# Performance work log

Hardware: AMD Instinct MI355X
Metric: run time of the kernel (lower is better)

## Reference

```python
import jax, jax.numpy as jnp
import numpy as np

NUM_STEPS = 50
NUM_DOF = 1
NVAR = NUM_STEPS * NUM_DOF
T = 0.05
V_MAX, A_MAX, J_MAX = 1.0, 2.0, 5.0
P_MAX = np.pi
THETA0 = 0.0
RHO = 1.0
MAXITER = 15
BATCH = 32768
HIDDEN = 1024
EPS = 1e-5


def _build_mats():
    # finite-difference operators (num_dof=1 so kron with eye(1) is identity)
    P_vel = np.eye(NUM_STEPS)
    P_acc = np.diff(P_vel, axis=0) / T          # (49, 50)
    P_jerk = np.diff(P_acc, axis=0) / T         # (48, 50)
    P_pos = np.cumsum(P_vel, axis=0) * T        # (50, 50)
    A_control = np.vstack([P_vel, -P_vel, P_acc, -P_acc,
                           P_jerk, -P_jerk, P_pos, -P_pos]).astype(np.float32)  # (394, 50)
    A_eq = np.zeros((2, NUM_STEPS), np.float32)
    A_eq[0, 0] = 1.0
    A_eq[1, -1] = 1.0
    cost = np.eye(NVAR) + RHO * A_control.T @ A_control
    Q = np.block([[cost, A_eq.T], [A_eq, np.zeros((2, 2))]])
    Q_inv = np.linalg.inv(Q).astype(np.float32)  # (52, 52)
    na = NUM_STEPS - 1
    nj = na - 1
    # limits used inside the iteration (p_max on both halves)
    b_iter = np.concatenate([np.full(2 * NUM_STEPS, V_MAX), np.full(2 * na, A_MAX),
                             np.full(2 * nj, J_MAX), np.full(2 * NUM_STEPS, P_MAX)]).astype(np.float32)
    # limits used for the slack init (p_max -/+ theta_init)
    b_init = np.concatenate([np.full(2 * NUM_STEPS, V_MAX), np.full(2 * na, A_MAX),
                             np.full(2 * nj, J_MAX), np.full(NUM_STEPS, P_MAX - THETA0),
                             np.full(NUM_STEPS, P_MAX + THETA0)]).astype(np.float32)
    return jnp.asarray(A_control), jnp.asarray(Q_inv), jnp.asarray(b_iter), jnp.asarray(b_init)


def _bn(x, g, b):
    # BatchNorm1d in training mode: biased batch statistics
    m = jnp.mean(x, axis=0)
    v = jnp.var(x, axis=0)
    return g * (x - m) * jax.lax.rsqrt(v + EPS) + b


def setup_inputs() -> dict:
    key = jax.random.key(0)
    ks = jax.random.split(key, 6)
    x = jax.random.normal(ks[0], (BATCH, NVAR), jnp.float32)
    W1 = jax.random.normal(ks[1], (NVAR, HIDDEN), jnp.float32) * 0.1
    W2 = jax.random.normal(ks[2], (HIDDEN, HIDDEN), jnp.float32) * 0.03
    W3 = jax.random.normal(ks[3], (HIDDEN, 256), jnp.float32) * 0.03
    W4 = jax.random.normal(ks[4], (256, 2 * NVAR), jnp.float32) * 0.06
    z = lambda n: jnp.zeros((n,), jnp.float32)
    o = lambda n: jnp.ones((n,), jnp.float32)
    return {"xi_samples_input_nn": x,
            "W1": W1, "b1": z(HIDDEN), "g1": o(HIDDEN), "be1": z(HIDDEN),
            "W2": W2, "b2": z(HIDDEN), "g2": o(HIDDEN), "be2": z(HIDDEN),
            "W3": W3, "b3": z(256), "g3": o(256), "be3": z(256),
            "W4": W4, "b4": z(2 * NVAR)}


def reference(xi_samples_input_nn, W1, b1, g1, be1, W2, b2, g2, be2,
              W3, b3, g3, be3, W4, b4):
    x = xi_samples_input_nn  # (B, nvar): both MLP input and projection target
    A_c, Q_inv, b_it, b_in = _build_mats()

    # MLP decoder
    h = jax.nn.relu(_bn(x @ W1 + b1, g1, be1))
    h = jax.nn.relu(_bn(h @ W2 + b2, g2, be2))
    h = jax.nn.relu(_bn(h @ W3 + b3, g3, be3))
    out = h @ W4 + b4                     # (B, 2*nvar)
    xi0 = out[:, :NVAR]
    lam0 = out[:, NVAR:2 * NVAR]

    s0 = jnp.maximum(0.0, b_in - xi0 @ A_c.T)        # (B, 394)
    b_eq = jnp.zeros((x.shape[0], 2), x.dtype)       # v_start = v_goal = 0

    def step(carry, _):
        xi, s, lam = carry
        b_aug = b_it - s
        # A_projection = I, so A_proj.T @ x.T -> x
        lincost = -lam - x - RHO * (b_aug @ A_c)
        rhs = jnp.concatenate([-lincost, b_eq], axis=1)   # (B, 52)
        sol = rhs @ Q_inv.T
        xi_n = sol[:, :NVAR]
        s_n = jnp.maximum(0.0, b_it - xi_n @ A_c.T)
        res = xi_n @ A_c.T - b_it + s_n
        res_norm = jnp.linalg.norm(res, axis=1)
        lam_n = lam - RHO * (res @ A_c)
        fp = (jnp.linalg.norm(xi - xi_n, axis=1)
              + jnp.linalg.norm(lam - lam_n, axis=1)
              + jnp.linalg.norm(s - s_n, axis=1))
        return (xi_n, s_n, lam_n), (res_norm, fp)

    (xi, s, lam), (primal, fixed_pt) = jax.lax.scan(step, (xi0, s0, lam0), None, length=MAXITER)
    avg_res_fixed_point = jnp.mean(fixed_pt, axis=0)  # (B,)
    avg_res_primal = jnp.mean(primal, axis=0)         # (B,)
    return xi, avg_res_fixed_point, avg_res_primal
```

## Files before the change

### kernel.cpp

```cpp
#include <hip/hip_runtime.h>
#include <math.h>

#define BATCH 32768
#define NVARS 50
#define H1 1024
#define H2 1024
#define H3 256
#define NOUT 100
#define EPSBN 1e-5f

#define TF   0.05f
#define AF   20.0f
#define JF   400.0f
#define VMAX 1.0f
#define AMAX 2.0f
#define JMAX 5.0f
#define PMAX 3.14159265358979323846f

typedef unsigned short ushort_t;
typedef __attribute__((ext_vector_type(8))) short short8;
typedef __attribute__((ext_vector_type(4))) float f32x4;

__device__ float g_z1[(size_t)BATCH * H1];
__device__ float g_z2[(size_t)BATCH * H2];
__device__ float g_ps[32 * 1024];
__device__ float g_pq[32 * 1024];
__device__ float g_scale[3 * 1024];
__device__ float g_shift[3 * 1024];
__device__ float g_Mp[2800];
__device__ float g_xT[(size_t)NVARS * BATCH];
__device__ float g_nnT[(size_t)NOUT * BATCH];
__device__ ushort_t g_w2p[(size_t)3 * H1 * H2];
__device__ ushort_t g_w3p[(size_t)3 * H2 * H3];

__device__ __forceinline__ void split3(float f, ushort_t& h, ushort_t& m, ushort_t& l)
{
    unsigned u = __float_as_uint(f);
    unsigned r = u + 0x7fffu + ((u >> 16) & 1u);
    h = (ushort_t)(r >> 16);
    float f1 = f - __uint_as_float((unsigned)h << 16);
    unsigned u1 = __float_as_uint(f1);
    unsigned r1 = u1 + 0x7fffu + ((u1 >> 16) & 1u);
    m = (ushort_t)(r1 >> 16);
    float f2 = f1 - __uint_as_float((unsigned)m << 16);
    unsigned u2 = __float_as_uint(f2);
    unsigned r2 = u2 + 0x7fffu + ((u2 >> 16) & 1u);
    l = (ushort_t)(r2 >> 16);
}

__global__ void build_M(float* __restrict__ Mout)
{
    __shared__ double aug[52][104];
    __shared__ int piv;
    int tid = threadIdx.x;

    const double Tf = (double)0.05f;
    const double c3[3] = { 400.0, -800.0, 400.0 };

    for (int idx = tid; idx < 52 * 104; idx += 64) {
        int j = idx / 104, k = idx % 104;
        double v = 0.0;
        if (k >= 52) {
            v = (k == 52 + j) ? 1.0 : 0.0;
        } else if (j < 50 && k < 50) {
            double q = (j == k) ? 3.0 : 0.0;
            if (j == k) q += 800.0 * ((j < 49 ? 1 : 0) + (j > 0 ? 1 : 0));
            if (j - k == 1 || k - j == 1) q += -800.0;
            int lo = j > k ? j : k; lo -= 2; if (lo < 0) lo = 0;
            int hi = j < k ? j : k; if (hi > 47) hi = 47;
            for (int i = lo; i <= hi; ++i) {
                int dj = j - i, dk = k - i;
                if (dj >= 0 && dj <= 2 && dk >= 0 && dk <= 2)
                    q += 2.0 * c3[dj] * c3[dk];
            }
            int mx = j > k ? j : k;
            q += 2.0 * Tf * Tf * (double)(50 - mx);
            v = q;
        } else if ((j == 50 && k == 0) || (j == 0 && k == 50) ||
                   (j == 51 && k == 49) || (j == 49 && k == 51)) {
            v = 1.0;
        }
        aug[j][k] = v;
    }
    __syncthreads();

    for (int c = 0; c < 52; ++c) {
        if (tid == 0) {
            int p = c; double best = fabs(aug[c][c]);
            for (int r = c + 1; r < 52; ++r) {
                double v = fabs(aug[r][c]);
                if (v > best) { best = v; p = r; }
            }
            piv = p;
        }
        __syncthreads();
        int p = piv;
        if (p != c) {
            for (int k = tid; k < 104; k += 64) {
                double t = aug[c][k]; aug[c][k] = aug[p][k]; aug[p][k] = t;
            }
        }
        __syncthreads();
        double pv = aug[c][c];
        __syncthreads();
        for (int k = tid; k < 104; k += 64) aug[c][k] /= pv;
        __syncthreads();
        if (tid < 52 && tid != c) {
            double f = aug[tid][c];
            for (int k = 0; k < 104; ++k) aug[tid][k] -= f * aug[c][k];
        }
        __syncthreads();
    }

    for (int idx = tid; idx < 2800; idx += 64) {
        int slot = idx % 28;
        int kk2 = idx / 28;
        int k = kk2 >> 1, par = kk2 & 1;
        int j = par * 25 + slot;
        Mout[idx] = (slot < 25) ? (float)aug[j][52 + k] : 0.f;
    }
}

template <int C>
__global__ __launch_bounds__(64)
void transp(const float* __restrict__ Z, float* __restrict__ ZT)
{
    __shared__ float t[64][C + 1];
    const int lane = threadIdx.x;
    const size_t r0 = (size_t)blockIdx.x * 64;
#pragma unroll 1
    for (int i = 0; i < C; ++i) {
        int idx = i * 64 + lane;
        int r = idx / C, c = idx % C;
        t[r][c] = Z[r0 * C + idx];
    }
    __syncthreads();
#pragma unroll 1
    for (int c = 0; c < C; ++c)
        ZT[(size_t)c * BATCH + r0 + lane] = t[lane][c];
}

__global__ __launch_bounds__(512)
void wsplit_pack(const float* __restrict__ W, ushort_t* __restrict__ Wp,
                 int K, int N)
{
    int t = threadIdx.x;
    int n0 = blockIdx.x * 16, k0 = blockIdx.y * 32;
    int kk = t >> 4, nn = t & 15;
    float f = W[(size_t)(k0 + kk) * N + n0 + nn];
    ushort_t h, m, l;
    split3(f, h, m, l);
    int Nsub = N >> 4;
    int lane = (kk >> 3) * 16 + nn, e = kk & 7;
    size_t base = ((size_t)((k0 >> 5) * Nsub + (n0 >> 4)) * 3) * 512 + lane * 8 + e;
    Wp[base]        = h;
    Wp[base + 512]  = m;
    Wp[base + 1024] = l;
}

__global__ __launch_bounds__(256)
void gemm_mfma(const float* __restrict__ A, const ushort_t* __restrict__ Wp,
               const float* __restrict__ bias,
               const float* __restrict__ scale, const float* __restrict__ shift,
               float* __restrict__ C, int M, int K, int N, int ntn)
{
    __shared__ __attribute__((aligned(16))) ushort_t lds[3][4][64][8];

    const int nwg = gridDim.x;
    const int chunk = nwg >> 3;
    const int b = blockIdx.x;
    const int logical = (b & 7) * chunk + (b >> 3);
    const int rowt = logical / ntn;
    const int colt = logical - rowt * ntn;
    const int row0 = rowt * 64;
    const int col0s = colt * 16;

    const int t = threadIdx.x;
    const int lane = t & 63, wn = t >> 6;
    const int fr = lane & 15, fg = lane >> 4;
    const int srow = t & 63, skc = t >> 6;
    const int Nsub = N >> 4;

    f32x4 acc[4][4];
#pragma unroll
    for (int m = 0; m < 4; ++m)
#pragma unroll
        for (int n = 0; n < 4; ++n)
#pragma unroll
            for (int q = 0; q < 4; ++q) acc[m][n][q] = 0.f;

    int ks = 0;
    for (int k0 = 0; k0 < K; k0 += 32, ++ks) {
        {
            const float* ap = A + (size_t)(row0 + srow) * K + k0 + skc * 8;
            float4 f0 = *(const float4*)ap;
            float4 f1 = *(const float4*)(ap + 4);
            const float* scp = scale + k0 + skc * 8;
            const float* shp = shift + k0 + skc * 8;
            float4 sc0 = *(const float4*)scp, sc1 = *(const float4*)(scp + 4);
            float4 sh0 = *(const float4*)shp, sh1 = *(const float4*)(shp + 4);
            float v[8];
            v[0] = fmaxf(f0.x * sc0.x + sh0.x, 0.f);
            v[1] = fmaxf(f0.y * sc0.y + sh0.y, 0.f);
            v[2] = fmaxf(f0.z * sc0.z + sh0.z, 0.f);
            v[3] = fmaxf(f0.w * sc0.w + sh0.w, 0.f);
            v[4] = fmaxf(f1.x * sc1.x + sh1.x, 0.f);
            v[5] = fmaxf(f1.y * sc1.y + sh1.y, 0.f);
            v[6] = fmaxf(f1.z * sc1.z + sh1.z, 0.f);
            v[7] = fmaxf(f1.w * sc1.w + sh1.w, 0.f);
            ushort_t h_[8], m_[8], l_[8];
#pragma unroll
            for (int q = 0; q < 8; ++q) split3(v[q], h_[q], m_[q], l_[q]);
#define PK(a,b2) (((unsigned)(a)) | (((unsigned)(b2)) << 16))
            *(uint4*)&lds[0][skc][srow][0] = make_uint4(PK(h_[0],h_[1]), PK(h_[2],h_[3]), PK(h_[4],h_[5]), PK(h_[6],h_[7]));
            *(uint4*)&lds[1][skc][srow][0] = make_uint4(PK(m_[0],m_[1]), PK(m_[2],m_[3]), PK(m_[4],m_[5]), PK(m_[6],m_[7]));
            *(uint4*)&lds[2][skc][srow][0] = make_uint4(PK(l_[0],l_[1]), PK(l_[2],l_[3]), PK(l_[4],l_[5]), PK(l_[6],l_[7]));
#undef PK
        }
        __syncthreads();

        short8 b_h[4], b_m[4], b_l[4];
#pragma unroll
        for (int n = 0; n < 4; ++n) {
            size_t base = ((size_t)(ks * Nsub + col0s + wn * 4 + n) * 3) * 512 + lane * 8;
            b_h[n] = *(const short8*)(Wp + base);
            b_m[n] = *(const short8*)(Wp + base + 512);
            b_l[n] = *(const short8*)(Wp + base + 1024);
        }
#pragma unroll
        for (int m = 0; m < 4; ++m) {
            int r = m * 16 + fr;
            short8 a_h = *(const short8*)&lds[0][fg][r][0];
            short8 a_m = *(const short8*)&lds[1][fg][r][0];
            short8 a_l = *(const short8*)&lds[2][fg][r][0];
#pragma unroll
            for (int n = 0; n < 4; ++n) {
                f32x4 c = acc[m][n];
                c = __builtin_amdgcn_mfma_f32_16x16x32_bf16(a_l, b_h[n], c, 0, 0, 0);
                c = __builtin_amdgcn_mfma_f32_16x16x32_bf16(a_h, b_l[n], c, 0, 0, 0);
                c = __builtin_amdgcn_mfma_f32_16x16x32_bf16(a_m, b_m[n], c, 0, 0, 0);
                c = __builtin_amdgcn_mfma_f32_16x16x32_bf16(a_m, b_h[n], c, 0, 0, 0);
                c = __builtin_amdgcn_mfma_f32_16x16x32_bf16(a_h, b_m[n], c, 0, 0, 0);
                c = __builtin_amdgcn_mfma_f32_16x16x32_bf16(a_h, b_h[n], c, 0, 0, 0);
                acc[m][n] = c;
            }
        }
        __syncthreads();
    }

#pragma unroll
    for (int m = 0; m < 4; ++m)
#pragma unroll
        for (int n = 0; n < 4; ++n) {
            int cc = (col0s + wn * 4 + n) * 16 + fr;
            float bv = bias[cc];
#pragma unroll
            for (int q = 0; q < 4; ++q) {
                int rr = row0 + m * 16 + fg * 4 + q;
                C[(size_t)rr * N + cc] = acc[m][n][q] + bv;
            }
        }
}

template <int BN_APPLY>
__global__ __launch_bounds__(256)
void gemm_k(const float* __restrict__ A, const float* __restrict__ W,
            const float* __restrict__ bias,
            const float* __restrict__ scale, const float* __restrict__ shift,
            float* __restrict__ C, int M, int K, int N)
{
    const int BM = 128, BN = 128, BK = 16;
    __shared__ __attribute__((aligned(16))) float As[BK][BM + 4];
    __shared__ __attribute__((aligned(16))) float Ws[BK][BN];
    int tid = threadIdx.x;
    int tm = tid >> 4, tn = tid & 15;
    int row0 = blockIdx.x * BM, col0 = blockIdx.y * BN;

    float acc[8][8];
#pragma unroll
    for (int i = 0; i < 8; ++i)
#pragma unroll
        for (int j = 0; j < 8; ++j) acc[i][j] = 0.f;

    int alr = tid >> 4;
    int alk = tid & 15;
    int wlc = tid & 127;
    int wlk = tid >> 7;

    for (int k0 = 0; k0 < K; k0 += BK) {
#pragma unroll
        for (int i = 0; i < 8; ++i) {
            int rr = row0 + alr + i * 16;
            int kk = k0 + alk;
            float v = 0.f;
            if (kk < K) {
                v = A[(size_t)rr * K + kk];
                if (BN_APPLY) v = fmaxf(v * scale[kk] + shift[kk], 0.f);
            }
            As[alk][alr + i * 16] = v;
        }
#pragma unroll
        for (int i = 0; i < 8; ++i) {
            int kk = k0 + wlk + i * 2;
            int cc = col0 + wlc;
            Ws[wlk + i * 2][wlc] = (kk < K && cc < N) ? W[(size_t)kk * N + cc] : 0.f;
        }
        __syncthreads();
#pragma unroll
        for (int kk = 0; kk < BK; ++kk) {
            float av[8], wv[8];
            float4 tv;
            tv = *(const float4*)&As[kk][tm * 8];     av[0]=tv.x; av[1]=tv.y; av[2]=tv.z; av[3]=tv.w;
            tv = *(const float4*)&As[kk][tm * 8 + 4]; av[4]=tv.x; av[5]=tv.y; av[6]=tv.z; av[7]=tv.w;
            tv = *(const float4*)&Ws[kk][tn * 8];     wv[0]=tv.x; wv[1]=tv.y; wv[2]=tv.z; wv[3]=tv.w;
            tv = *(const float4*)&Ws[kk][tn * 8 + 4]; wv[4]=tv.x; wv[5]=tv.y; wv[6]=tv.z; wv[7]=tv.w;
#pragma unroll
            for (int i = 0; i < 8; ++i)
#pragma unroll
                for (int j = 0; j < 8; ++j) acc[i][j] += av[i] * wv[j];
        }
        __syncthreads();
    }
#pragma unroll
    for (int i = 0; i < 8; ++i) {
        int rr = row0 + tm * 8 + i;
#pragma unroll
        for (int j = 0; j < 8; ++j) {
            int cc = col0 + tn * 8 + j;
            if (cc < N) C[(size_t)rr * N + cc] = acc[i][j] + bias[cc];
        }
    }
}

__global__ __launch_bounds__(256)
void stats_part(const float* __restrict__ Z, float* __restrict__ ps,
                float* __restrict__ pq, int M, int C, int chunks)
{
    int lc = threadIdx.x & 63;
    int col = blockIdx.x * 64 + lc;
    int rg = threadIdx.x >> 6;
    int rpc = M / chunks;
    int r0 = blockIdx.y * rpc;
    float s = 0.f, q = 0.f;
    for (int rr = r0 + rg; rr < r0 + rpc; rr += 4) {
        float v = Z[(size_t)rr * C + col];
        s += v; q += v * v;
    }
    __shared__ float ls[4][64], lq[4][64];
    ls[rg][lc] = s; lq[rg][lc] = q;
    __syncthreads();
    if (rg == 0) {
        float S = ls[0][lc] + ls[1][lc] + ls[2][lc] + ls[3][lc];
        float Q = lq[0][lc] + lq[1][lc] + lq[2][lc] + lq[3][lc];
        ps[(size_t)blockIdx.y * C + col] = S;
        pq[(size_t)blockIdx.y * C + col] = Q;
    }
}

__global__ void stats_fin(const float* __restrict__ ps, const float* __restrict__ pq,
                          const float* __restrict__ g, const float* __restrict__ be,
                          float* __restrict__ scale, float* __restrict__ shift,
                          int C, int M, int chunks)
{
    int c = blockIdx.x * blockDim.x + threadIdx.x;
    if (c >= C) return;
    float S = 0.f, Q = 0.f;
    for (int i = 0; i < chunks; ++i) { S += ps[(size_t)i * C + c]; Q += pq[(size_t)i * C + c]; }
    float inv = 1.0f / (float)M;
    float mean = S * inv;
    float var = Q * inv - mean * mean;
    float rstd = 1.0f / sqrtf(var + EPSBN);
    float sc = g[c] * rstd;
    scale[c] = sc;
    shift[c] = be[c] - mean * sc;
}

__global__ __launch_bounds__(64, 1)
void iter_k(const float* __restrict__ XT, const float* __restrict__ NNT,
            const float* __restrict__ Mp, float* __restrict__ out)
{
    __shared__ float sA[50 * 32];
    __shared__ float sB[50 * 32];
    __shared__ float sLam[50 * 32];
    __shared__ float sXv[50 * 32];
    __shared__ float sRh[50 * 32];
    const int lane = threadIdx.x;
    const int r = lane >> 1, par = lane & 1;
    const int base = blockIdx.x * 32;
    const int row = base + r;
#define IDX2(k) (((k) << 5) + r)

#pragma unroll 1
    for (int idx = lane; idx < 1600; idx += 64) {
        int k = idx >> 5, rr = idx & 31;
        sA[idx]   = NNT[(size_t)k * BATCH + base + rr];
        sLam[idx] = NNT[(size_t)(50 + k) * BATCH + base + rr];
        sXv[idx]  = XT[(size_t)k * BATCH + base + rr];
    }
    float* cx = sA;
    float* cn = sB;
    float fps = 0.f, prs = 0.f;
    float rh[50];
    const float* mp = Mp + par * 28;

#pragma unroll 1
    for (int it = 0; it < 15; ++it) {
#pragma unroll
        for (int k = 0; k < 50; ++k) rh[k] = 0.f;
        {
            float pre = 0.f, Sp = 0.f, ap = 0.f;
            float xc = cx[IDX2(0)];
#pragma unroll
            for (int k = 0; k < 50; ++k) {
                float xn = (k < 49) ? cx[IDX2(k + 1)] : 0.f;
                rh[k] += fminf(VMAX, xc) - fminf(VMAX, -xc);
                rh[k] -= TF * Sp;
                pre += xc;
                float p = TF * pre;
                Sp += fminf(PMAX, p) - fminf(PMAX, -p);
                if (k < 49) {
                    float a = AF * (xn - xc);
                    float da = fminf(AMAX, a) - fminf(AMAX, -a);
                    rh[k] -= AF * da; rh[k + 1] += AF * da;
                    if (k >= 1) {
                        float j = AF * (a - ap);
                        float dj = fminf(JMAX, j) - fminf(JMAX, -j);
                        rh[k - 1] += JF * dj; rh[k] -= 2.f * JF * dj; rh[k + 1] += JF * dj;
                    }
                    ap = a;
                }
                xc = xn;
            }
            float Stot = TF * Sp;
#pragma unroll
            for (int k = 0; k < 50; ++k)
                sRh[IDX2(k)] = rh[k] + sLam[IDX2(k)] + sXv[IDX2(k)] + Stot;
        }

        {
            float xr[28];
#pragma unroll
            for (int jj = 0; jj < 28; ++jj) xr[jj] = 0.f;
#pragma unroll 2
            for (int k = 0; k < 50; ++k) {
                float rv = sRh[IDX2(k)];
                const float4* m4 = (const float4*)(mp + k * 56);
#pragma unroll
                for (int q = 0; q < 7; ++q) {
                    float4 mv = m4[q];
                    xr[q * 4 + 0] += mv.x * rv;
                    xr[q * 4 + 1] += mv.y * rv;
                    xr[q * 4 + 2] += mv.z * rv;
                    xr[q * 4 + 3] += mv.w * rv;
                }
            }
#pragma unroll
            for (int jj = 0; jj < 25; ++jj)
                cn[((par * 25 + jj) << 5) + r] = xr[jj];
        }

        float res2 = 0.f, ds2 = 0.f, dxi2 = 0.f, dlam2 = 0.f;
#pragma unroll
        for (int k = 0; k < 50; ++k) rh[k] = 0.f;
        {
            float preo = 0.f, pren = 0.f, SpF = 0.f, aop = 0.f, anp = 0.f;
            float xoc = cx[IDX2(0)], xnc = cn[IDX2(0)];
#pragma unroll
            for (int k = 0; k < 50; ++k) {
                float xon = (k < 49) ? cx[IDX2(k + 1)] : 0.f;
                float xnn = (k < 49) ? cn[IDX2(k + 1)] : 0.f;
                float d = xoc - xnc; dxi2 += d * d;
                float rp = fmaxf(xnc - VMAX, 0.f), rm = fmaxf(-xnc - VMAX, 0.f);
                res2 += rp * rp + rm * rm;
                float so = fmaxf(VMAX - xoc, 0.f), sn = fmaxf(VMAX - xnc, 0.f);
                d = so - sn; ds2 += d * d;
                so = fmaxf(VMAX + xoc, 0.f); sn = fmaxf(VMAX + xnc, 0.f);
                d = so - sn; ds2 += d * d;
                rh[k] += rp - rm;
                rh[k] -= TF * SpF;
                preo += xoc; pren += xnc;
                float po = TF * preo, pn = TF * pren;
                rp = fmaxf(pn - PMAX, 0.f); rm = fmaxf(-pn - PMAX, 0.f);
                res2 += rp * rp + rm * rm;
                so = fmaxf(PMAX - po, 0.f); sn = fmaxf(PMAX - pn, 0.f);
                d = so - sn; ds2 += d * d;
                so = fmaxf(PMAX + po, 0.f); sn = fmaxf(PMAX + pn, 0.f);
                d = so - sn; ds2 += d * d;
                SpF += rp - rm;
                if (k < 49) {
                    float ao = AF * (xon - xoc), an = AF * (xnn - xnc);
                    rp = fmaxf(an - AMAX, 0.f); rm = fmaxf(-an - AMAX, 0.f);
                    res2 += rp * rp + rm * rm;
                    so = fmaxf(AMAX - ao, 0.f); sn = fmaxf(AMAX - an, 0.f);
                    d = so - sn; ds2 += d * d;
                    so = fmaxf(AMAX + ao, 0.f); sn = fmaxf(AMAX + an, 0.f);
                    d = so - sn; ds2 += d * d;
                    float fa = rp - rm; rh[k] -= AF * fa; rh[k + 1] += AF * fa;
                    if (k >= 1) {
                        float jo = AF * (ao - aop), jn = AF * (an - anp);
                        rp = fmaxf(jn - JMAX, 0.f); rm = fmaxf(-jn - JMAX, 0.f);
                        res2 += rp * rp + rm * rm;
                        so = fmaxf(JMAX - jo, 0.f); sn = fmaxf(JMAX - jn, 0.f);
                        d = so - sn; ds2 += d * d;
                        so = fmaxf(JMAX + jo, 0.f); sn = fmaxf(JMAX + jn, 0.f);
                        d = so - sn; ds2 += d * d;
                        float fj = rp - rm;
                        rh[k - 1] += JF * fj; rh[k] -= 2.f * JF * fj; rh[k + 1] += JF * fj;
                    }
                    aop = ao; anp = an;
                }
                xoc = xon; xnc = xnn;
            }
            float SF = TF * SpF;
#pragma unroll
            for (int k = 0; k < 50; ++k) {
                float gk = rh[k] + SF;
                dlam2 += gk * gk;
                sLam[IDX2(k)] -= gk;
            }
        }
        prs += sqrtf(res2);
        fps += sqrtf(dxi2) + sqrtf(dlam2) + sqrtf(ds2);
        float* tp = cx; cx = cn; cn = tp;
    }
#pragma unroll 1
    for (int idx = lane; idx < 1600; idx += 64) {
        int rr = idx / 50, kk = idx - rr * 50;
        out[(size_t)(base + rr) * 50 + kk] = cx[(kk << 5) + rr];
    }
    out[(size_t)BATCH * 50 + row] = fps * (1.f / 15.f);
    out[(size_t)BATCH * 51 + row] = prs * (1.f / 15.f);
#undef IDX2
}

extern "C" void kernel_launch(void* const* d_in, const int* in_sizes, int n_in,
                              void* d_out, int out_size, void* d_ws, size_t ws_size,
                              hipStream_t stream)
{
    const float* x   = (const float*)d_in[0];
    const float* W1  = (const float*)d_in[1];
    const float* b1  = (const float*)d_in[2];
    const float* g1  = (const float*)d_in[3];
    const float* be1 = (const float*)d_in[4];
    const float* W2  = (const float*)d_in[5];
    const float* b2  = (const float*)d_in[6];
    const float* g2  = (const float*)d_in[7];
    const float* be2 = (const float*)d_in[8];
    const float* W3  = (const float*)d_in[9];
    const float* b3  = (const float*)d_in[10];
    const float* g3  = (const float*)d_in[11];
    const float* be3 = (const float*)d_in[12];
    const float* W4  = (const float*)d_in[13];
    const float* b4  = (const float*)d_in[14];

    float *z1, *z2, *ps, *pq, *scb, *shb, *Mp, *xT, *nnT;
    ushort_t *w2p, *w3p;
    hipGetSymbolAddress((void**)&z1,  HIP_SYMBOL(g_z1));
    hipGetSymbolAddress((void**)&z2,  HIP_SYMBOL(g_z2));
    hipGetSymbolAddress((void**)&ps,  HIP_SYMBOL(g_ps));
    hipGetSymbolAddress((void**)&pq,  HIP_SYMBOL(g_pq));
    hipGetSymbolAddress((void**)&scb, HIP_SYMBOL(g_scale));
    hipGetSymbolAddress((void**)&shb, HIP_SYMBOL(g_shift));
    hipGetSymbolAddress((void**)&Mp,  HIP_SYMBOL(g_Mp));
    hipGetSymbolAddress((void**)&xT,  HIP_SYMBOL(g_xT));
    hipGetSymbolAddress((void**)&nnT, HIP_SYMBOL(g_nnT));
    hipGetSymbolAddress((void**)&w2p, HIP_SYMBOL(g_w2p));
    hipGetSymbolAddress((void**)&w3p, HIP_SYMBOL(g_w3p));

    float* z3  = z1;
    float* nno = z1 + (size_t)BATCH * H3;
    float* sc1 = scb;        float* sh1 = shb;
    float* sc2 = scb + 1024; float* sh2 = shb + 1024;
    float* sc3 = scb + 2048; float* sh3 = shb + 2048;

    dim3 blk(256);
    hipLaunchKernelGGL(build_M, dim3(1), dim3(64), 0, stream, Mp);
    hipLaunchKernelGGL(wsplit_pack, dim3(H2 / 16, H1 / 32), dim3(512), 0, stream, W2, w2p, H1, H2);
    hipLaunchKernelGGL(wsplit_pack, dim3(H3 / 16, H2 / 32), dim3(512), 0, stream, W3, w3p, H2, H3);
    hipLaunchKernelGGL((transp<50>), dim3(BATCH / 64), dim3(64), 0, stream, x, xT);

    hipLaunchKernelGGL((gemm_k<0>), dim3(BATCH / 128, H1 / 128), blk, 0, stream,
                       x, W1, b1, (const float*)nullptr, (const float*)nullptr,
                       z1, BATCH, NVARS, H1);
    hipLaunchKernelGGL(stats_part, dim3(H1 / 64, 32), blk, 0, stream, z1, ps, pq, BATCH, H1, 32);
    hipLaunchKernelGGL(stats_fin, dim3(4), dim3(256), 0, stream, ps, pq, g1, be1, sc1, sh1, H1, BATCH, 32);
    hipLaunchKernelGGL(gemm_mfma, dim3((BATCH / 64) * (H2 / 256)), blk, 0, stream,
                       z1, w2p, b2, sc1, sh1, z2, BATCH, H1, H2, H2 / 256);
    hipLaunchKernelGGL(stats_part, dim3(H2 / 64, 32), blk, 0, stream, z2, ps, pq, BATCH, H2, 32);
    hipLaunchKernelGGL(stats_fin, dim3(4), dim3(256), 0, stream, ps, pq, g2, be2, sc2, sh2, H2, BATCH, 32);
    hipLaunchKernelGGL(gemm_mfma, dim3((BATCH / 64) * (H3 / 256)), blk, 0, stream,
                       z2, w3p, b3, sc2, sh2, z3, BATCH, H2, H3, H3 / 256);
    hipLaunchKernelGGL(stats_part, dim3(H3 / 64, 32), blk, 0, stream, z3, ps, pq, BATCH, H3, 32);
    hipLaunchKernelGGL(stats_fin, dim3(1), dim3(256), 0, stream, ps, pq, g3, be3, sc3, sh3, H3, BATCH, 32);
    hipLaunchKernelGGL((gemm_k<1>), dim3(BATCH / 128, 1), blk, 0, stream,
                       z3, W4, b4, sc3, sh3, nno, BATCH, H3, NOUT);
    hipLaunchKernelGGL((transp<100>), dim3(BATCH / 64), dim3(64), 0, stream, nno, nnT);
    hipLaunchKernelGGL(iter_k, dim3(BATCH / 32), dim3(64), 0, stream,
                       xT, nnT, Mp, (float*)d_out);
}
```

Measured before the change: 1.758 ms.

## Double-buffer LDS A tiles in split-bf16 MFMA GEMM with register prefetch

The A-tile staging buffer in LDS is doubled. The next K-slice of A is loaded into registers before the MFMA block runs, and it is split and written into the alternate buffer afterwards. This lets global-load latency overlap with matrix-core work and removes one of the two barriers per K-step. In exchange, LDS use doubles (from 12 KB to 24 KB per block) and the prefetched values take extra registers, which may reduce occupancy.

```diff
diff --git a/kernel.cpp b/kernel.cpp
--- a/kernel.cpp
+++ b/kernel.cpp
@@ -164,7 +164,7 @@
                const float* __restrict__ scale, const float* __restrict__ shift,
                float* __restrict__ C, int M, int K, int N, int ntn)
 {
-    __shared__ __attribute__((aligned(16))) ushort_t lds[3][4][64][8];
+    __shared__ __attribute__((aligned(16))) ushort_t lds[2][3][4][64][8];
 
     const int nwg = gridDim.x;
     const int chunk = nwg >> 3;
@@ -180,6 +180,7 @@
     const int fr = lane & 15, fg = lane >> 4;
     const int srow = t & 63, skc = t >> 6;
     const int Nsub = N >> 4;
+    const int nk = K >> 5;
 
     f32x4 acc[4][4];
 #pragma unroll
@@ -189,35 +190,55 @@
 #pragma unroll
             for (int q = 0; q < 4; ++q) acc[m][n][q] = 0.f;
 
-    int ks = 0;
-    for (int k0 = 0; k0 < K; k0 += 32, ++ks) {
-        {
-            const float* ap = A + (size_t)(row0 + srow) * K + k0 + skc * 8;
-            float4 f0 = *(const float4*)ap;
-            float4 f1 = *(const float4*)(ap + 4);
-            const float* scp = scale + k0 + skc * 8;
-            const float* shp = shift + k0 + skc * 8;
-            float4 sc0 = *(const float4*)scp, sc1 = *(const float4*)(scp + 4);
-            float4 sh0 = *(const float4*)shp, sh1 = *(const float4*)(shp + 4);
-            float v[8];
-            v[0] = fmaxf(f0.x * sc0.x + sh0.x, 0.f);
-            v[1] = fmaxf(f0.y * sc0.y + sh0.y, 0.f);
-            v[2] = fmaxf(f0.z * sc0.z + sh0.z, 0.f);
-            v[3] = fmaxf(f0.w * sc0.w + sh0.w, 0.f);
-            v[4] = fmaxf(f1.x * sc1.x + sh1.x, 0.f);
-            v[5] = fmaxf(f1.y * sc1.y + sh1.y, 0.f);
-            v[6] = fmaxf(f1.z * sc1.z + sh1.z, 0.f);
-            v[7] = fmaxf(f1.w * sc1.w + sh1.w, 0.f);
-            ushort_t h_[8], m_[8], l_[8];
-#pragma unroll
-            for (int q = 0; q < 8; ++q) split3(v[q], h_[q], m_[q], l_[q]);
-#define PK(a,b2) (((unsigned)(a)) | (((unsigned)(b2)) << 16))
-            *(uint4*)&lds[0][skc][srow][0] = make_uint4(PK(h_[0],h_[1]), PK(h_[2],h_[3]), PK(h_[4],h_[5]), PK(h_[6],h_[7]));
-            *(uint4*)&lds[1][skc][srow][0] = make_uint4(PK(m_[0],m_[1]), PK(m_[2],m_[3]), PK(m_[4],m_[5]), PK(m_[6],m_[7]));
-            *(uint4*)&lds[2][skc][srow][0] = make_uint4(PK(l_[0],l_[1]), PK(l_[2],l_[3]), PK(l_[4],l_[5]), PK(l_[6],l_[7]));
-#undef PK
-        }
-        __syncthreads();
+    const float* arow = A + (size_t)(row0 + srow) * K + skc * 8;
+
+#define SPLIT_WRITE(BUF, F0, F1, KOFF)                                         \
+    {                                                                          \
+        const float* scp = scale + (KOFF) + skc * 8;                           \
+        const float* shp = shift + (KOFF) + skc * 8;                           \
+        float4 sc0 = *(const float4*)scp, sc1 = *(const float4*)(scp + 4);     \
+        float4 sh0 = *(const float4*)shp, sh1 = *(const float4*)(shp + 4);     \
+        float v[8];                                                            \
+        v[0] = fmaxf((F0).x * sc0.x + sh0.x, 0.f);                             \
+        v[1] = fmaxf((F0).y * sc0.y + sh0.y, 0.f);                             \
+        v[2] = fmaxf((F0).z * sc0.z + sh0.z, 0.f);                             \
+        v[3] = fmaxf((F0).w * sc0.w + sh0.w, 0.f);                             \
+        v[4] = fmaxf((F1).x * sc1.x + sh1.x, 0.f);                             \
+        v[5] = fmaxf((F1).y * sc1.y + sh1.y, 0.f);                             \
+        v[6] = fmaxf((F1).z * sc1.z + sh1.z, 0.f);                             \
+        v[7] = fmaxf((F1).w * sc1.w + sh1.w, 0.f);                             \
+        ushort_t h_[8], m_[8], l_[8];                                          \
+        _Pragma("unroll")                                                      \
+        for (int q = 0; q < 8; ++q) split3(v[q], h_[q], m_[q], l_[q]);         \
+        *(uint4*)&lds[BUF][0][skc][srow][0] = make_uint4(                      \
+            (unsigned)h_[0] | ((unsigned)h_[1] << 16),                         \
+            (unsigned)h_[2] | ((unsigned)h_[3] << 16),                         \
+            (unsigned)h_[4] | ((unsigned)h_[5] << 16),                         \
+            (unsigned)h_[6] | ((unsigned)h_[7] << 16));                        \
+        *(uint4*)&lds[BUF][1][skc][srow][0] = make_uint4(                      \
+            (unsigned)m_[0] | ((unsigned)m_[1] << 16),                         \
+            (unsigned)m_[2] | ((unsigned)m_[3] << 16),                         \
+            (unsigned)m_[4] | ((unsigned)m_[5] << 16),                         \
+            (unsigned)m_[6] | ((unsigned)m_[7] << 16));                        \
+        *(uint4*)&lds[BUF][2][skc][srow][0] = make_uint4(                      \
+            (unsigned)l_[0] | ((unsigned)l_[1] << 16),                         \
+            (unsigned)l_[2] | ((unsigned)l_[3] << 16),                         \
+            (unsigned)l_[4] | ((unsigned)l_[5] << 16),                         \
+            (unsigned)l_[6] | ((unsigned)l_[7] << 16));                        \
+    }
+
+    {
+        float4 f0 = *(const float4*)(arow);
+        float4 f1 = *(const float4*)(arow + 4);
+        SPLIT_WRITE(0, f0, f1, 0)
+    }
+    __syncthreads();
+
+    int cur = 0;
+    for (int ks = 0; ks < nk; ++ks) {
+        int kn = (ks + 1 < nk) ? (ks + 1) : ks;
+        float4 f0 = *(const float4*)(arow + kn * 32);
+        float4 f1 = *(const float4*)(arow + kn * 32 + 4);
 
         short8 b_h[4], b_m[4], b_l[4];
 #pragma unroll
@@ -230,9 +251,9 @@
 #pragma unroll
         for (int m = 0; m < 4; ++m) {
             int r = m * 16 + fr;
-            short8 a_h = *(const short8*)&lds[0][fg][r][0];
-            short8 a_m = *(const short8*)&lds[1][fg][r][0];
-            short8 a_l = *(const short8*)&lds[2][fg][r][0];
+            short8 a_h = *(const short8*)&lds[cur][0][fg][r][0];
+            short8 a_m = *(const short8*)&lds[cur][1][fg][r][0];
+            short8 a_l = *(const short8*)&lds[cur][2][fg][r][0];
 #pragma unroll
             for (int n = 0; n < 4; ++n) {
                 f32x4 c = acc[m][n];
@@ -245,8 +266,13 @@
                 acc[m][n] = c;
             }
         }
-        __syncthreads();
-    }
+        if (ks + 1 < nk) {
+            SPLIT_WRITE(cur ^ 1, f0, f1, (ks + 1) * 32)
+        }
+        __syncthreads();
+        cur ^= 1;
+    }
+#undef SPLIT_WRITE
 
 #pragma unroll
     for (int m = 0; m < 4; ++m)
```

After: 1.701 ms. -3.2%, faster.
